# Kernel optimization log

Hardware: AMD Instinct MI355X
Metric: run time of the kernel (lower is better)

The kernel has to match this reference:

```python
import jax, jax.numpy as jnp
import numpy as np

U = 1024   # units
DK = 1024  # attention inner dim (dk)
B, T, D = 64, 128, 256


def setup_inputs() -> dict:
    key = jax.random.key(0)
    ks = jax.random.split(key, 20)
    s_w = 0.02   # dense-kernel init scale
    s_a = 0.03   # ~glorot for (1, dk) attention vectors
    inp = {
        'x': jax.random.normal(ks[0], (B, T, D), jnp.float32),
        'kernel': jax.random.normal(ks[1], (D, 5 * U), jnp.float32) * s_w,
        'recurrent_kernel': jax.random.normal(ks[2], (U, 5 * U), jnp.float32) * s_w,
        'cell_kernel': jax.random.normal(ks[3], (U, 5 * U), jnp.float32) * s_w,
        'bias': jnp.zeros((5 * U,), jnp.float32),
        'aggregation': jax.random.normal(ks[4], (3 * U, U), jnp.float32) * s_w,
    }
    att_names = ['up_att_downl', 'up_att_downr', 'up_att_randl', 'up_att_randr',
                 'rand_att_upl', 'rand_att_upr', 'rand_att_downl', 'rand_att_downr',
                 'down_att_upl', 'down_att_upr', 'down_att_randl', 'down_att_randr']
    for i, n in enumerate(att_names):
        inp[n] = jax.random.normal(ks[5 + i], (1, DK), jnp.float32) * s_a
    return inp


def _cumsoftmax_l2r(x):
    return jnp.cumsum(jax.nn.softmax(x, axis=-1), axis=-1)


def _cumsoftmax_r2l(x):
    # reverse, softmax+cumsum, reverse back (softmax is permutation-equivariant)
    return jnp.cumsum(jax.nn.softmax(x, axis=-1)[..., ::-1], axis=-1)[..., ::-1]


def _forward(x, kernel, recurrent_kernel, cell_kernel, bias, aggregation,
             up_att_downl, up_att_downr, up_att_randl, up_att_randr,
             rand_att_upl, rand_att_upr, rand_att_downl, rand_att_downr,
             down_att_upl, down_att_upr, down_att_randl, down_att_randr):
    # Rank-1 collapse of (v w_l)(u w_r)^T v chains: scalar = w_l . w_r
    s_ud = jnp.sum(up_att_downl * up_att_downr)
    s_ur = jnp.sum(up_att_randl * up_att_randr)
    s_ru = jnp.sum(rand_att_upl * rand_att_upr)
    s_rd = jnp.sum(rand_att_downl * rand_att_downr)
    s_du = jnp.sum(down_att_upl * down_att_upr)
    s_dr = jnp.sum(down_att_randl * down_att_randr)

    # precompute input projection for all timesteps: [T, B, 5U]
    xw = jnp.einsum('btd,dk->tbk', x, kernel) + bias

    def step(carry, xw_t):
        c, h = carry
        z = xw_t + h @ recurrent_kernel + c @ cell_kernel  # [B, 5U]
        up = _cumsoftmax_l2r(z[:, :U])
        down = _cumsoftmax_r2l(z[:, U:2 * U])
        rand = z[:, 2 * U:3 * U]
        du = jnp.sum(down * up, axis=-1, keepdims=True)    # <down, up> per batch
        ru = jnp.sum(rand * up, axis=-1, keepdims=True)
        dr = jnp.sum(down * rand, axis=-1, keepdims=True)
        O1 = jax.nn.sigmoid(s_ud * up * du) + jax.nn.sigmoid(s_ur * up * ru)
        O2 = jax.nn.sigmoid(s_ru * rand * ru) + jax.nn.sigmoid(s_rd * rand * dr)
        O3 = jax.nn.sigmoid(s_du * down * du) + jax.nn.sigmoid(s_dr * down * dr)
        f_gate = jax.nn.sigmoid(jnp.concatenate([O1, O2, O3], axis=-1) @ aggregation)
        i_gate = 1.0 - f_gate
        o_gate = z[:, 3 * U:4 * U]          # NOTE: no sigmoid in the original
        c_in = jnp.tanh(z[:, 4 * U:])
        c_new = f_gate * c + i_gate * c_in
        h_new = o_gate * jnp.tanh(c_new)
        return (c_new, h_new), h_new

    init = (jnp.zeros((x.shape[0], U), x.dtype), jnp.zeros((x.shape[0], U), x.dtype))
    _, hs = jax.lax.scan(step, init, xw)
    return jnp.transpose(hs, (1, 0, 2))  # return_sequences=True -> [B, T, U]


def reference(x, kernel, recurrent_kernel, cell_kernel, bias, aggregation,
              up_att_downl, up_att_downr, up_att_randl, up_att_randr,
              rand_att_upl, rand_att_upr, rand_att_downl, rand_att_downr,
              down_att_upl, down_att_upr, down_att_randl, down_att_randr):
    return _forward(x, kernel, recurrent_kernel, cell_kernel, bias, aggregation,
                    up_att_downl, up_att_downr, up_att_randl, up_att_randr,
                    rand_att_upl, rand_att_upr, rand_att_downl, rand_att_downr,
                    down_att_upl, down_att_upr, down_att_randl, down_att_randr)
```

## Files before the change

### kernel.cpp

```cpp
#include <hip/hip_runtime.h>
#include <hip/hip_bf16.h>


typedef short  bf16x8 __attribute__((ext_vector_type(8)));
typedef float  f32x4  __attribute__((ext_vector_type(4)));
typedef _Float16 f16;
typedef _Float16 f16x8 __attribute__((ext_vector_type(8)));
typedef __hip_bfloat16 bf16;
typedef unsigned long long u64;

#define U 1024
#define BATCH 64
#define TSTEPS 128
#define DIM 256
#define N5 5120
#define K2 2048

#define OFF_WRC   0u
#define OFF_KT    20971520u
#define OFF_AGGT  23592960u
#define OFF_XBF   29884416u
#define OFF_ZP    34078720u
#define OFF_ABUF  39321600u
#define OFF_C32   39845888u
#define OFF_OBUF  40108032u
#define OFF_SCAL  40501248u
#define OFF_CTR   40501504u
#define OFF_PB    OFF_KT

#define NBLK_A 160
#define NBLK_B 64
#define NBLK   224
#define FPAD   8

#define KT_OFF 131072

#define MFMA16(a,b,c)  __builtin_amdgcn_mfma_f32_16x16x32_bf16((a),(b),(c),0,0,0)
#define MFMA16H(a,b,c) __builtin_amdgcn_mfma_f32_16x16x32_f16((a),(b),(c),0,0,0)

__global__ __launch_bounds__(256) void k_xconv(const float* __restrict__ in,
                                               f16* __restrict__ o, int n4) {
    const int i = blockIdx.x * 256 + threadIdx.x;
    if (i < n4) {
        const float4 v = ((const float4*)in)[i];
        f16 tmp[4] = {(f16)v.x, (f16)v.y, (f16)v.z, (f16)v.w};
        ((uint2*)o)[i] = *(const uint2*)tmp;
    }
}

__global__ __launch_bounds__(256) void k_transpose_h(const float* __restrict__ in,
                                                     f16* __restrict__ out,
                                                     int C, int out_stride, int out_off) {
    __shared__ f16 tile[64][65];
    const int tc = blockIdx.x * 64, tr = blockIdx.y * 64;
    const int tx = threadIdx.x & 63, ty0 = threadIdx.x >> 6;
#pragma unroll
    for (int i = 0; i < 64; i += 4)
        tile[ty0 + i][tx] = (f16)(in[(tr + ty0 + i) * C + tc + tx]);
    __syncthreads();
#pragma unroll
    for (int i = 0; i < 64; i += 4)
        out[(tc + ty0 + i) * out_stride + out_off + tr + tx] = tile[tx][ty0 + i];
}

__global__ __launch_bounds__(256) void k_transpose_b(const float* __restrict__ in,
                                                     bf16* __restrict__ out,
                                                     int C, int out_stride, int out_off) {
    __shared__ bf16 tile[64][65];
    const int tc = blockIdx.x * 64, tr = blockIdx.y * 64;
    const int tx = threadIdx.x & 63, ty0 = threadIdx.x >> 6;
#pragma unroll
    for (int i = 0; i < 64; i += 4)
        tile[ty0 + i][tx] = __float2bfloat16(in[(tr + ty0 + i) * C + tc + tx]);
    __syncthreads();
#pragma unroll
    for (int i = 0; i < 64; i += 4)
        out[(tc + ty0 + i) * out_stride + out_off + tr + tx] = tile[tx][ty0 + i];
}

struct AttPtrs { const float* p[12]; };

__global__ __launch_bounds__(256) void k_scal(AttPtrs ap, float* __restrict__ scal) {
    __shared__ float red[256];
    const int tid = threadIdx.x;
    for (int q = 0; q < 6; ++q) {
        const float* l = ap.p[2 * q];
        const float* r = ap.p[2 * q + 1];
        float s = 0.f;
        for (int i = tid; i < 1024; i += 256)
            s += l[i] * r[i];
        red[tid] = s; __syncthreads();
        for (int o = 128; o > 0; o >>= 1) {
            if (tid < o) red[tid] += red[tid + o];
            __syncthreads();
        }
        if (tid == 0) scal[q] = red[0];
        __syncthreads();
    }
}

__device__ __forceinline__ float wave_sum(float v) {
#pragma unroll
    for (int o = 32; o > 0; o >>= 1) v += __shfl_xor(v, o, 64);
    return v;
}
__device__ __forceinline__ float wave_max(float v) {
#pragma unroll
    for (int o = 32; o > 0; o >>= 1) v = fmaxf(v, __shfl_xor(v, o, 64));
    return v;
}
__device__ __forceinline__ float wave_scan(float v, int lane) {
#pragma unroll
    for (int o = 1; o < 64; o <<= 1) {
        float n = __shfl_up(v, o, 64);
        if (lane >= o) v += n;
    }
    return v;
}
__device__ __forceinline__ float block_sum(float v, float* sm4, int w, int lane) {
    float s = wave_sum(v);
    if (lane == 0) sm4[w] = s;
    __syncthreads();
    float r = sm4[0] + sm4[1] + sm4[2] + sm4[3];
    __syncthreads();
    return r;
}
__device__ __forceinline__ float block_max(float v, float* sm4, int w, int lane) {
    float s = wave_max(v);
    if (lane == 0) sm4[w] = s;
    __syncthreads();
    float r = fmaxf(fmaxf(sm4[0], sm4[1]), fmaxf(sm4[2], sm4[3]));
    __syncthreads();
    return r;
}
__device__ __forceinline__ float block_scan(float v, float* sm4, int w, int lane, float* total) {
    float ws = wave_scan(v, lane);
    if (lane == 63) sm4[w] = ws;
    __syncthreads();
    float base = 0.f;
    if (w > 0) base += sm4[0];
    if (w > 1) base += sm4[1];
    if (w > 2) base += sm4[2];
    *total = sm4[0] + sm4[1] + sm4[2] + sm4[3];
    __syncthreads();
    return base + ws;
}
__device__ __forceinline__ float sigm(float x) { return 1.f / (1.f + __expf(-x)); }

__device__ __forceinline__ u64 ald64(const void* p) {
    return __hip_atomic_load((const u64*)p, __ATOMIC_RELAXED, __HIP_MEMORY_SCOPE_AGENT);
}
__device__ __forceinline__ bf16x8 ald16B(const bf16* p) {
    union { bf16x8 v; u64 u[2]; } r;
    r.u[0] = ald64(p);
    r.u[1] = ald64((const char*)p + 8);
    return r.v;
}
__device__ __forceinline__ f16x8 aldh16B(const f16* p) {
    union { f16x8 v; u64 u[2]; } r;
    r.u[0] = ald64(p);
    r.u[1] = ald64((const char*)p + 8);
    return r.v;
}
__device__ __forceinline__ f32x4 ald_f4(const float* p) {
    union { f32x4 v; u64 u[2]; } r;
    r.u[0] = ald64(p);
    r.u[1] = ald64(p + 2);
    return r.v;
}
__device__ __forceinline__ float ald_f(const float* p) {
    return __hip_atomic_load(p, __ATOMIC_RELAXED, __HIP_MEMORY_SCOPE_AGENT);
}
__device__ __forceinline__ void ast64(void* p, u64 v) {
    __hip_atomic_store((u64*)p, v, __ATOMIC_RELAXED, __HIP_MEMORY_SCOPE_AGENT);
}
__device__ __forceinline__ void ast32(void* p, unsigned v) {
    __hip_atomic_store((unsigned*)p, v, __ATOMIC_RELAXED, __HIP_MEMORY_SCOPE_AGENT);
}
__device__ __forceinline__ void ast_f(float* p, float v) {
    __hip_atomic_store(p, v, __ATOMIC_RELAXED, __HIP_MEMORY_SCOPE_AGENT);
}
__device__ __forceinline__ unsigned h16bits(f16 h) {
    unsigned short s; __builtin_memcpy(&s, &h, 2); return (unsigned)s;
}
__device__ __forceinline__ u64 packf2(float a, float b) {
    union { float f[2]; u64 u; } r; r.f[0] = a; r.f[1] = b; return r.u;
}

__device__ __forceinline__ void signal_flag(int* f, int v) {
    __syncthreads();
    if (threadIdx.x == 0)
        __hip_atomic_store(f, v, __ATOMIC_RELAXED, __HIP_MEMORY_SCOPE_AGENT);
}
__device__ __forceinline__ void wait_ge(const int* f, int n, int tgt) {
    if (threadIdx.x < 64) {
        for (;;) {
            int mn = 0x7fffffff;
            for (int i = threadIdx.x; i < n; i += 64) {
                const int v = __hip_atomic_load(f + i * FPAD, __ATOMIC_RELAXED,
                                                __HIP_MEMORY_SCOPE_AGENT);
                mn = v < mn ? v : mn;
            }
            if (__all(mn >= tgt)) break;
            __builtin_amdgcn_s_sleep(1);
        }
    }
    __syncthreads();
}

__device__ __forceinline__ bf16x8 lds_rd(const char* s, int nloc, int kb, int rs) {
    return *(const bf16x8*)(s + nloc * rs + (kb ^ ((nloc & 7) << 4)));
}
__device__ __forceinline__ f16x8 lds_rdh(const char* s, int nloc, int kb, int rs) {
    return *(const f16x8*)(s + nloc * rs + (kb ^ ((nloc & 7) << 4)));
}

__global__ __launch_bounds__(256, 1) void k_persist(
    const f16* __restrict__ xbf, const f16* __restrict__ kt,
    const f16* __restrict__ wrct, const bf16* __restrict__ aggt,
    float* __restrict__ zp, f16* __restrict__ abuf,
    float* __restrict__ c32, bf16* __restrict__ obuf,
    float* __restrict__ pbuf,
    const float* __restrict__ scal, const float* __restrict__ bias,
    float* __restrict__ out, int* __restrict__ ctr)
{
    __shared__ __align__(16) char smem[147456];
    __shared__ float sm4[4];

    const int bid = blockIdx.x, tid = threadIdx.x;
    const int w = tid >> 6, lane = tid & 63;
    const int ml = lane & 15, q = lane >> 4;
    int* fA = ctr;
    int* fB = ctr + 1280;
    int* fC = ctr + 1792;
    int* fP = ctr + 2304;

    if (bid < NBLK_A) {
        const int cg = bid >> 2;
        const int kq = bid & 3;
        const int n0 = cg * 128;
        const int kwbase = (kq < 2) ? kq * 512 : 1024 + (kq - 2) * 512;
        const int kA0 = (kq & 1) * 512;

        for (int i = 0; i < 32; ++i) {
            const int cid = i * 256 + tid;
            const int row = cid >> 6, k = (cid & 63) * 8;
            f16x8 v = *(const f16x8*)(wrct + (size_t)(n0 + row) * K2 + kwbase + k);
            *(f16x8*)(smem + row * 1024 + ((k * 2) ^ ((row & 7) << 4))) = v;
        }
        for (int i = 0; i < 4; ++i) {
            const int cid = i * 256 + tid;
            const int row = cid >> 3, k = (cid & 7) * 8;
            f16x8 v = *(const f16x8*)(kt + (size_t)(n0 + row) * DIM + kq * 64 + k);
            *(f16x8*)(smem + KT_OFF + row * 128 + ((k * 2) ^ ((row & 7) << 4))) = v;
        }
        __syncthreads();

        const int arow = w * 16 + ml;
        const f16* hP = abuf + (kq < 2 ? 0 : 1) * 65536 + arow * U + kA0;
        const f16* xrow = xbf + (size_t)arow * TSTEPS * DIM;
        float* zpq = zp + (size_t)kq * 64 * N5;
        int* fCmy = fC + ((kq & 1) * 32) * FPAD;

        for (int t = 0; t < TSTEPS; ++t) {
            const f16x8 ax0 = *(const f16x8*)(xrow + t * DIM + kq * 64 + q * 8);
            const f16x8 ax1 = *(const f16x8*)(xrow + t * DIM + kq * 64 + 32 + q * 8);

            wait_ge(fCmy, 32, t);

            f16x8 a[16];
#pragma unroll
            for (int i = 0; i < 16; ++i)
                a[i] = aldh16B(hP + i * 32 + q * 8);

            f32x4 acc[8];
#pragma unroll
            for (int i = 0; i < 8; ++i) acc[i] = (f32x4){0.f, 0.f, 0.f, 0.f};

#pragma unroll
            for (int cx = 0; cx < 2; ++cx) {
                const f16x8 axv = cx ? ax1 : ax0;
#pragma unroll
                for (int ct = 0; ct < 8; ++ct) {
                    const f16x8 b = lds_rdh(smem + KT_OFF, ct * 16 + ml, cx * 64 + q * 16, 128);
                    acc[ct] = MFMA16H(axv, b, acc[ct]);
                }
            }

#pragma unroll
            for (int i = 0; i < 16; ++i) {
                const int g = i >> 1, c = i & 1;
#pragma unroll
                for (int ct = 0; ct < 8; ++ct) {
                    const f16x8 b = lds_rdh(smem, ct * 16 + ml,
                                            g * 128 + c * 64 + q * 16, 1024);
                    acc[ct] = MFMA16H(a[i], b, acc[ct]);
                }
            }

#pragma unroll
            for (int ct = 0; ct < 8; ++ct)
#pragma unroll
                for (int r = 0; r < 4; ++r) {
                    const float v = acc[ct][r];
                    const float pv = __shfl_xor(v, 1, 64);
                    if (!(ml & 1)) {
                        const int row = w * 16 + q * 4 + r;
                        const int col = n0 + ct * 16 + ml;
                        ast64(&zpq[row * N5 + col], packf2(v, pv));
                    }
                }
            signal_flag(fA + bid * FPAD, t + 1);
        }
    } else {
        const int rb = bid - NBLK_A;
        const int cg = rb >> 2;
        const int kq2 = rb & 3;
        const int nst = cg * 64 + kq2 * 16;
        const int KO = kq2 * 768;

        for (int i = 0; i < 24; ++i) {
            const int cid = i * 256 + tid;
            const int nloc = cid / 96, kc = cid - nloc * 96;
            const int k = kc * 8;
            bf16x8 v = *(const bf16x8*)(aggt + (size_t)(cg * 64 + nloc) * 3072 + KO + k);
            *(bf16x8*)(smem + nloc * 1536 + ((k * 2) ^ ((nloc & 7) << 4))) = v;
        }
        __syncthreads();

        const float s_ud = scal[0], s_ur = scal[1], s_ru = scal[2],
                    s_rd = scal[3], s_du = scal[4], s_dr = scal[5];
        const int rowA = w * 16 + ml;
        const bf16* orow = obuf + rowA * 3072 + KO;
        float* cpriv = c32 + rb * 1024;

        for (int t = 0; t < TSTEPS; ++t) {
            wait_ge(fA, 96, t + 1);
            {
                f32x4 zu = {0.f,0.f,0.f,0.f}, zd = {0.f,0.f,0.f,0.f}, zn = {0.f,0.f,0.f,0.f};
#pragma unroll
                for (int kqi = 0; kqi < 4; ++kqi) {
                    const float* bp = zp + (size_t)kqi * 64 * N5 + rb * N5;
                    zu += ald_f4(bp + tid * 4);
                    zd += ald_f4(bp + U + tid * 4);
                    zn += ald_f4(bp + 2 * U + tid * 4);
                }
                zu += ((const f32x4*)bias)[tid];
                zd += ((const f32x4*)(bias + U))[tid];
                zn += ((const f32x4*)(bias + 2 * U))[tid];

                float mup = block_max(fmaxf(fmaxf(zu[0], zu[1]), fmaxf(zu[2], zu[3])), sm4, w, lane);
                const float e0 = __expf(zu[0] - mup), e1 = __expf(zu[1] - mup),
                            e2 = __expf(zu[2] - mup), e3 = __expf(zu[3] - mup);
                float totu;
                float inclu = block_scan(e0 + e1 + e2 + e3, sm4, w, lane, &totu);
                const float exclu = inclu - (e0 + e1 + e2 + e3);
                const float inv_u = 1.f / totu;
                const float u0 = (exclu + e0) * inv_u;
                const float u1 = (exclu + e0 + e1) * inv_u;
                const float u2 = (exclu + e0 + e1 + e2) * inv_u;
                const float u3 = (exclu + e0 + e1 + e2 + e3) * inv_u;

                float mdn = block_max(fmaxf(fmaxf(zd[0], zd[1]), fmaxf(zd[2], zd[3])), sm4, w, lane);
                const float f0 = __expf(zd[0] - mdn), f1 = __expf(zd[1] - mdn),
                            f2 = __expf(zd[2] - mdn), f3 = __expf(zd[3] - mdn);
                float totd;
                float incld = block_scan(f0 + f1 + f2 + f3, sm4, w, lane, &totd);
                const float excld = incld - (f0 + f1 + f2 + f3);
                const float inv_d = 1.f / totd;
                const float d0 = (totd - excld) * inv_d;
                const float d1 = (totd - excld - f0) * inv_d;
                const float d2 = (totd - excld - f0 - f1) * inv_d;
                const float d3 = (totd - excld - f0 - f1 - f2) * inv_d;

                const float du = block_sum(d0 * u0 + d1 * u1 + d2 * u2 + d3 * u3, sm4, w, lane);
                const float ru = block_sum(zn[0] * u0 + zn[1] * u1 + zn[2] * u2 + zn[3] * u3, sm4, w, lane);
                const float dr = block_sum(d0 * zn[0] + d1 * zn[1] + d2 * zn[2] + d3 * zn[3], sm4, w, lane);

                bf16* orw = obuf + rb * 3072;
                const int j0 = tid * 4;
                const float uu[4] = {u0, u1, u2, u3};
                const float dd[4] = {d0, d1, d2, d3};
                const float rr[4] = {zn[0], zn[1], zn[2], zn[3]};
                union { bf16 h[4]; u64 u; } p1, p2, p3;
#pragma unroll
                for (int i = 0; i < 4; ++i) {
                    p1.h[i] = __float2bfloat16(sigm(s_ud * uu[i] * du) + sigm(s_ur * uu[i] * ru));
                    p2.h[i] = __float2bfloat16(sigm(s_ru * rr[i] * ru) + sigm(s_rd * rr[i] * dr));
                    p3.h[i] = __float2bfloat16(sigm(s_du * dd[i] * du) + sigm(s_dr * dd[i] * dr));
                }
                ast64(orw + j0,         p1.u);
                ast64(orw + U + j0,     p2.u);
                ast64(orw + 2 * U + j0, p3.u);
            }
            signal_flag(fB + rb * FPAD, t + 1);

            wait_ge(fA + 96 * FPAD, 64, t + 1);
            float z3v[4], z4v[4];
            {
                const int col = nst + ml;
                const int r0 = w * 16 + q * 4;
#pragma unroll
                for (int r = 0; r < 4; ++r) {
                    z3v[r] = bias[3 * U + col];
                    z4v[r] = bias[4 * U + col];
#pragma unroll
                    for (int kqi = 0; kqi < 4; ++kqi) {
                        const float* zr = zp + (size_t)kqi * 64 * N5 + (size_t)(r0 + r) * N5;
                        z3v[r] += ald_f(zr + 3 * U + col);
                        z4v[r] += ald_f(zr + 4 * U + col);
                    }
                }
            }
            wait_ge(fB, NBLK_B, t + 1);
            {
                f32x4 acc[4];
#pragma unroll
                for (int i = 0; i < 4; ++i) acc[i] = (f32x4){0.f, 0.f, 0.f, 0.f};
                bf16x8 ob[3][8];
#pragma unroll
                for (int G = 0; G < 3; ++G)
#pragma unroll
                    for (int j = 0; j < 8; ++j)
                        ob[G][j] = ald16B(orow + (G * 8 + j) * 32 + q * 8);
#pragma unroll
                for (int g = 0; g < 3; ++g)
#pragma unroll
                    for (int j = 0; j < 8; ++j) {
                        const int kc = g * 8 + j;
#pragma unroll
                        for (int ct = 0; ct < 4; ++ct) {
                            const bf16x8 b = lds_rd(smem, ct * 16 + ml, kc * 64 + q * 16, 1536);
                            acc[ct] = MFMA16(ob[g][j], b, acc[ct]);
                        }
                    }
#pragma unroll
                for (int ct = 0; ct < 4; ++ct)
#pragma unroll
                    for (int r = 0; r < 4; ++r) {
                        const int row = w * 16 + q * 4 + r;
                        ast_f(&pbuf[(((size_t)cg * 64 + row) * 64 + ct * 16 + ml) * 4 + kq2],
                              acc[ct][r]);
                    }
            }
            signal_flag(fP + rb * FPAD, t + 1);
            wait_ge(fP + cg * 4 * FPAD, 4, t + 1);
            float hns[4];
            {
                const int col = nst + ml;
                const int r0 = w * 16 + q * 4;
#pragma unroll
                for (int r = 0; r < 4; ++r) {
                    const int row = r0 + r;
                    const f32x4 pj = ald_f4(&pbuf[(((size_t)cg * 64 + row) * 64 + kq2 * 16 + ml) * 4]);
                    const float s = (pj[0] + pj[1]) + (pj[2] + pj[3]);
                    const float f = sigm(s);
                    const float cold = cpriv[row * 16 + ml];
                    const float cn = f * cold + (1.f - f) * tanhf(z4v[r]);
                    const float hn = z3v[r] * tanhf(cn);
                    cpriv[row * 16 + ml] = cn;
                    hns[r] = hn;
                    const f16 hhb = (f16)hn;
                    const f16 ccb = (f16)cn;
                    unsigned vh = h16bits(hhb), vc = h16bits(ccb);
                    const unsigned ph = (unsigned)__shfl_xor((int)vh, 1, 64);
                    const unsigned pc = (unsigned)__shfl_xor((int)vc, 1, 64);
                    if (!(ml & 1)) {
                        const int eo = row * U + col;
                        ast32((unsigned*)(abuf + 0 * 65536 + eo), vh | (ph << 16));
                        ast32((unsigned*)(abuf + 1 * 65536 + eo), vc | (pc << 16));
                    }
                }
            }
            signal_flag(fC + rb * FPAD, t + 1);
            {
                const int col = nst + ml;
                const int r0 = w * 16 + q * 4;
#pragma unroll
                for (int r = 0; r < 4; ++r)
                    out[((size_t)(r0 + r) * TSTEPS + t) * U + col] = hns[r];
            }
        }
    }
}

extern "C" void kernel_launch(void* const* d_in, const int* in_sizes, int n_in,
                              void* d_out, int out_size, void* d_ws, size_t ws_size,
                              hipStream_t stream) {
    (void)in_sizes; (void)n_in; (void)out_size; (void)ws_size;
    const float* x    = (const float*)d_in[0];
    const float* Wk   = (const float*)d_in[1];
    const float* Wr   = (const float*)d_in[2];
    const float* Wc   = (const float*)d_in[3];
    const float* bias = (const float*)d_in[4];
    const float* agg  = (const float*)d_in[5];

    char* ws = (char*)d_ws;
    f16*   wrct = (f16*)(ws + OFF_WRC);
    f16*   kt   = (f16*)(ws + OFF_KT);
    bf16*  aggt = (bf16*)(ws + OFF_AGGT);
    f16*   xbf  = (f16*)(ws + OFF_XBF);
    float* zp   = (float*)(ws + OFF_ZP);
    f16*   abuf = (f16*)(ws + OFF_ABUF);
    float* c32  = (float*)(ws + OFF_C32);
    bf16*  obuf = (bf16*)(ws + OFF_OBUF);
    float* pbuf = (float*)(ws + OFF_PB);
    float* scal = (float*)(ws + OFF_SCAL);
    int*   ctr  = (int*)(ws + OFF_CTR);
    float* out  = (float*)d_out;

    hipMemsetAsync(abuf, 0, 2 * 65536 * sizeof(f16), stream);
    hipMemsetAsync(c32, 0, BATCH * U * sizeof(float), stream);
    hipMemsetAsync(ctr, 0, 12288, stream);

    k_xconv<<<(BATCH * TSTEPS * DIM / 4 + 255) / 256, 256, 0, stream>>>(x, xbf, BATCH * TSTEPS * DIM / 4);
    k_transpose_h<<<dim3(5120 / 64, 1024 / 64), 256, 0, stream>>>(Wr, wrct, 5120, 2048, 0);
    k_transpose_h<<<dim3(5120 / 64, 1024 / 64), 256, 0, stream>>>(Wc, wrct, 5120, 2048, 1024);
    k_transpose_h<<<dim3(5120 / 64, 256 / 64),  256, 0, stream>>>(Wk, kt,   5120, 256, 0);
    k_transpose_b<<<dim3(1024 / 64, 3072 / 64), 256, 0, stream>>>(agg, aggt, 1024, 3072, 0);

    AttPtrs ap;
    for (int i = 0; i < 12; ++i) ap.p[i] = (const float*)d_in[6 + i];
    k_scal<<<1, 256, 0, stream>>>(ap, scal);

    k_persist<<<NBLK, 256, 0, stream>>>(xbf, kt, wrct, aggt, zp, abuf, c32,
                                        obuf, pbuf, scal, bias, out, ctr);
}
```

Baseline: 3.363 ms.

## Remove split-K partial buffer for aggregation GEMM; each block owns full K for 16 columns

The aggregation matmul used to split K four ways across blocks, write partials to a global buffer, then run a second grid-level flag wait before summing them. Now each B-block keeps all 3072 K rows for its 16 output columns in LDS and computes the whole dot product itself, using two accumulators and a rotating register prefetch of obuf. Each wave waits only on the 16 producer flags for its own rows rather than on all blocks. This removes one global round trip and one cross-block barrier per timestep, at the cost of a larger serial MFMA chain and more obuf loads per block.

```diff
diff --git a/kernel.cpp b/kernel.cpp
--- a/kernel.cpp
+++ b/kernel.cpp
@@ -26,13 +26,13 @@
 #define OFF_OBUF  40108032u
 #define OFF_SCAL  40501248u
 #define OFF_CTR   40501504u
-#define OFF_PB    OFF_KT
 
 #define NBLK_A 160
 #define NBLK_B 64
 #define NBLK   224
 #define FPAD   8
 
+#define RS_B 6144
 #define KT_OFF 131072
 
 #define MFMA16(a,b,c)  __builtin_amdgcn_mfma_f32_16x16x32_bf16((a),(b),(c),0,0,0)
@@ -177,9 +177,6 @@
 __device__ __forceinline__ void ast32(void* p, unsigned v) {
     __hip_atomic_store((unsigned*)p, v, __ATOMIC_RELAXED, __HIP_MEMORY_SCOPE_AGENT);
 }
-__device__ __forceinline__ void ast_f(float* p, float v) {
-    __hip_atomic_store(p, v, __ATOMIC_RELAXED, __HIP_MEMORY_SCOPE_AGENT);
-}
 __device__ __forceinline__ unsigned h16bits(f16 h) {
     unsigned short s; __builtin_memcpy(&s, &h, 2); return (unsigned)s;
 }
@@ -207,6 +204,19 @@
     }
     __syncthreads();
 }
+__device__ __forceinline__ void wave_wait_ge(const int* f, int n, int tgt) {
+    const int lane = threadIdx.x & 63;
+    for (;;) {
+        int mn = 0x7fffffff;
+        for (int i = lane; i < n; i += 64) {
+            const int v = __hip_atomic_load(f + i * FPAD, __ATOMIC_RELAXED,
+                                            __HIP_MEMORY_SCOPE_AGENT);
+            mn = v < mn ? v : mn;
+        }
+        if (__all(mn >= tgt)) break;
+        __builtin_amdgcn_s_sleep(1);
+    }
+}
 
 __device__ __forceinline__ bf16x8 lds_rd(const char* s, int nloc, int kb, int rs) {
     return *(const bf16x8*)(s + nloc * rs + (kb ^ ((nloc & 7) << 4)));
@@ -220,7 +230,6 @@
     const f16* __restrict__ wrct, const bf16* __restrict__ aggt,
     float* __restrict__ zp, f16* __restrict__ abuf,
     float* __restrict__ c32, bf16* __restrict__ obuf,
-    float* __restrict__ pbuf,
     const float* __restrict__ scal, const float* __restrict__ bias,
     float* __restrict__ out, int* __restrict__ ctr)
 {
@@ -233,7 +242,6 @@
     int* fA = ctr;
     int* fB = ctr + 1280;
     int* fC = ctr + 1792;
-    int* fP = ctr + 2304;
 
     if (bid < NBLK_A) {
         const int cg = bid >> 2;
@@ -314,25 +322,26 @@
         }
     } else {
         const int rb = bid - NBLK_A;
-        const int cg = rb >> 2;
-        const int kq2 = rb & 3;
-        const int nst = cg * 64 + kq2 * 16;
-        const int KO = kq2 * 768;
-
+        const int n0b = rb * 16;
         for (int i = 0; i < 24; ++i) {
             const int cid = i * 256 + tid;
-            const int nloc = cid / 96, kc = cid - nloc * 96;
+            const int nloc = cid / 384, kc = cid - nloc * 384;
             const int k = kc * 8;
-            bf16x8 v = *(const bf16x8*)(aggt + (size_t)(cg * 64 + nloc) * 3072 + KO + k);
-            *(bf16x8*)(smem + nloc * 1536 + ((k * 2) ^ ((nloc & 7) << 4))) = v;
+            bf16x8 v = *(const bf16x8*)(aggt + (size_t)(n0b + nloc) * 3072 + k);
+            *(bf16x8*)(smem + nloc * RS_B + ((k * 2) ^ ((nloc & 7) << 4))) = v;
         }
         __syncthreads();
 
         const float s_ud = scal[0], s_ur = scal[1], s_ru = scal[2],
                     s_rd = scal[3], s_du = scal[4], s_dr = scal[5];
         const int rowA = w * 16 + ml;
-        const bf16* orow = obuf + rowA * 3072 + KO;
+        const bf16* orow = obuf + rowA * 3072;
         float* cpriv = c32 + rb * 1024;
+
+#define LOADO(G, BUF) do { _Pragma("unroll") \
+        for (int j_ = 0; j_ < 8; ++j_) \
+            ob[BUF][j_] = ald16B(orow + ((G) * 8 + j_) * 32 + q * 8); \
+        } while (0)
 
         for (int t = 0; t < TSTEPS; ++t) {
             wait_ge(fA, 96, t + 1);
@@ -398,7 +407,7 @@
             wait_ge(fA + 96 * FPAD, 64, t + 1);
             float z3v[4], z4v[4];
             {
-                const int col = nst + ml;
+                const int col = n0b + ml;
                 const int r0 = w * 16 + q * 4;
 #pragma unroll
                 for (int r = 0; r < 4; ++r) {
@@ -412,49 +421,33 @@
                     }
                 }
             }
-            wait_ge(fB, NBLK_B, t + 1);
-            {
-                f32x4 acc[4];
-#pragma unroll
-                for (int i = 0; i < 4; ++i) acc[i] = (f32x4){0.f, 0.f, 0.f, 0.f};
-                bf16x8 ob[3][8];
-#pragma unroll
-                for (int G = 0; G < 3; ++G)
-#pragma unroll
-                    for (int j = 0; j < 8; ++j)
-                        ob[G][j] = ald16B(orow + (G * 8 + j) * 32 + q * 8);
-#pragma unroll
-                for (int g = 0; g < 3; ++g)
-#pragma unroll
-                    for (int j = 0; j < 8; ++j) {
-                        const int kc = g * 8 + j;
-#pragma unroll
-                        for (int ct = 0; ct < 4; ++ct) {
-                            const bf16x8 b = lds_rd(smem, ct * 16 + ml, kc * 64 + q * 16, 1536);
-                            acc[ct] = MFMA16(ob[g][j], b, acc[ct]);
-                        }
-                    }
-#pragma unroll
-                for (int ct = 0; ct < 4; ++ct)
-#pragma unroll
-                    for (int r = 0; r < 4; ++r) {
-                        const int row = w * 16 + q * 4 + r;
-                        ast_f(&pbuf[(((size_t)cg * 64 + row) * 64 + ct * 16 + ml) * 4 + kq2],
-                              acc[ct][r]);
-                    }
-            }
-            signal_flag(fP + rb * FPAD, t + 1);
-            wait_ge(fP + cg * 4 * FPAD, 4, t + 1);
+            wave_wait_ge(fB + (w * 16) * FPAD, 16, t + 1);
             float hns[4];
             {
-                const int col = nst + ml;
+                f32x4 p0 = {0.f, 0.f, 0.f, 0.f}, p1 = {0.f, 0.f, 0.f, 0.f};
+                bf16x8 ob[4][8];
+                LOADO(0, 0);
+                LOADO(1, 1);
+                LOADO(2, 2);
+#pragma unroll
+                for (int g = 0; g < 12; ++g) {
+                    if (g < 9) LOADO(g + 3, (g + 3) & 3);
+#pragma unroll
+                    for (int j = 0; j < 8; ++j) {
+                        const int ch = g * 8 + j;
+                        const int kb = ch * 64 + q * 16;
+                        const bf16x8 b = lds_rd(smem, ml, kb, RS_B);
+                        if (j & 1) p1 = MFMA16(ob[g & 3][j], b, p1);
+                        else       p0 = MFMA16(ob[g & 3][j], b, p0);
+                    }
+                }
+                const f32x4 accv = p0 + p1;
+                const int col = n0b + ml;
                 const int r0 = w * 16 + q * 4;
 #pragma unroll
                 for (int r = 0; r < 4; ++r) {
                     const int row = r0 + r;
-                    const f32x4 pj = ald_f4(&pbuf[(((size_t)cg * 64 + row) * 64 + kq2 * 16 + ml) * 4]);
-                    const float s = (pj[0] + pj[1]) + (pj[2] + pj[3]);
-                    const float f = sigm(s);
+                    const float f = sigm(accv[r]);
                     const float cold = cpriv[row * 16 + ml];
                     const float cn = f * cold + (1.f - f) * tanhf(z4v[r]);
                     const float hn = z3v[r] * tanhf(cn);
@@ -474,13 +467,14 @@
             }
             signal_flag(fC + rb * FPAD, t + 1);
             {
-                const int col = nst + ml;
+                const int col = n0b + ml;
                 const int r0 = w * 16 + q * 4;
 #pragma unroll
                 for (int r = 0; r < 4; ++r)
                     out[((size_t)(r0 + r) * TSTEPS + t) * U + col] = hns[r];
             }
         }
+#undef LOADO
     }
 }
 
@@ -504,7 +498,6 @@
     f16*   abuf = (f16*)(ws + OFF_ABUF);
     float* c32  = (float*)(ws + OFF_C32);
     bf16*  obuf = (bf16*)(ws + OFF_OBUF);
-    float* pbuf = (float*)(ws + OFF_PB);
     float* scal = (float*)(ws + OFF_SCAL);
     int*   ctr  = (int*)(ws + OFF_CTR);
     float* out  = (float*)d_out;
@@ -524,5 +517,5 @@
     k_scal<<<1, 256, 0, stream>>>(ap, scal);
 
     k_persist<<<NBLK, 256, 0, stream>>>(xbf, kt, wrct, aggt, zp, abuf, c32,
-                                        obuf, pbuf, scal, bias, out, ctr);
-}
+                                        obuf, scal, bias, out, ctr);
+}
```

New measurement: 5.672 ms. 68.6% more time.

## Store inter-block partial sums in fp16 and merge the two A-stage waits

Applied to the files above, without the earlier changes.

Moves the inter-block partial buffers (z partials, aggregation partials, attention outputs) and the aggregation weights from fp32/bf16 to fp16, with fp16 MFMA for the aggregation matmul. This halves the global traffic through the synchronising buffers on the per-timestep critical path. The B blocks now wait once for all A blocks and load the output and cell-input gate partials early, instead of waiting separately on a second group. The cost is lower precision in the partial sums and a wider single wait, which may lose some overlap.

```diff
diff --git a/kernel.cpp b/kernel.cpp
--- a/kernel.cpp
+++ b/kernel.cpp
@@ -2,11 +2,9 @@
 #include <hip/hip_bf16.h>
 
 
-typedef short  bf16x8 __attribute__((ext_vector_type(8)));
 typedef float  f32x4  __attribute__((ext_vector_type(4)));
 typedef _Float16 f16;
 typedef _Float16 f16x8 __attribute__((ext_vector_type(8)));
-typedef __hip_bfloat16 bf16;
 typedef unsigned long long u64;
 
 #define U 1024
@@ -35,7 +33,6 @@
 
 #define KT_OFF 131072
 
-#define MFMA16(a,b,c)  __builtin_amdgcn_mfma_f32_16x16x32_bf16((a),(b),(c),0,0,0)
 #define MFMA16H(a,b,c) __builtin_amdgcn_mfma_f32_16x16x32_f16((a),(b),(c),0,0,0)
 
 __global__ __launch_bounds__(256) void k_xconv(const float* __restrict__ in,
@@ -57,21 +54,6 @@
 #pragma unroll
     for (int i = 0; i < 64; i += 4)
         tile[ty0 + i][tx] = (f16)(in[(tr + ty0 + i) * C + tc + tx]);
-    __syncthreads();
-#pragma unroll
-    for (int i = 0; i < 64; i += 4)
-        out[(tc + ty0 + i) * out_stride + out_off + tr + tx] = tile[tx][ty0 + i];
-}
-
-__global__ __launch_bounds__(256) void k_transpose_b(const float* __restrict__ in,
-                                                     bf16* __restrict__ out,
-                                                     int C, int out_stride, int out_off) {
-    __shared__ bf16 tile[64][65];
-    const int tc = blockIdx.x * 64, tr = blockIdx.y * 64;
-    const int tx = threadIdx.x & 63, ty0 = threadIdx.x >> 6;
-#pragma unroll
-    for (int i = 0; i < 64; i += 4)
-        tile[ty0 + i][tx] = __float2bfloat16(in[(tr + ty0 + i) * C + tc + tx]);
     __syncthreads();
 #pragma unroll
     for (int i = 0; i < 64; i += 4)
@@ -150,11 +132,8 @@
 __device__ __forceinline__ u64 ald64(const void* p) {
     return __hip_atomic_load((const u64*)p, __ATOMIC_RELAXED, __HIP_MEMORY_SCOPE_AGENT);
 }
-__device__ __forceinline__ bf16x8 ald16B(const bf16* p) {
-    union { bf16x8 v; u64 u[2]; } r;
-    r.u[0] = ald64(p);
-    r.u[1] = ald64((const char*)p + 8);
-    return r.v;
+__device__ __forceinline__ unsigned ald32(const void* p) {
+    return __hip_atomic_load((const unsigned*)p, __ATOMIC_RELAXED, __HIP_MEMORY_SCOPE_AGENT);
 }
 __device__ __forceinline__ f16x8 aldh16B(const f16* p) {
     union { f16x8 v; u64 u[2]; } r;
@@ -162,29 +141,21 @@
     r.u[1] = ald64((const char*)p + 8);
     return r.v;
 }
-__device__ __forceinline__ f32x4 ald_f4(const float* p) {
-    union { f32x4 v; u64 u[2]; } r;
-    r.u[0] = ald64(p);
-    r.u[1] = ald64(p + 2);
-    return r.v;
-}
-__device__ __forceinline__ float ald_f(const float* p) {
-    return __hip_atomic_load(p, __ATOMIC_RELAXED, __HIP_MEMORY_SCOPE_AGENT);
-}
 __device__ __forceinline__ void ast64(void* p, u64 v) {
     __hip_atomic_store((u64*)p, v, __ATOMIC_RELAXED, __HIP_MEMORY_SCOPE_AGENT);
 }
 __device__ __forceinline__ void ast32(void* p, unsigned v) {
     __hip_atomic_store((unsigned*)p, v, __ATOMIC_RELAXED, __HIP_MEMORY_SCOPE_AGENT);
 }
-__device__ __forceinline__ void ast_f(float* p, float v) {
-    __hip_atomic_store(p, v, __ATOMIC_RELAXED, __HIP_MEMORY_SCOPE_AGENT);
+__device__ __forceinline__ void ast16(void* p, unsigned short v) {
+    __hip_atomic_store((unsigned short*)p, v, __ATOMIC_RELAXED, __HIP_MEMORY_SCOPE_AGENT);
 }
 __device__ __forceinline__ unsigned h16bits(f16 h) {
     unsigned short s; __builtin_memcpy(&s, &h, 2); return (unsigned)s;
 }
-__device__ __forceinline__ u64 packf2(float a, float b) {
-    union { float f[2]; u64 u; } r; r.f[0] = a; r.f[1] = b; return r.u;
+__device__ __forceinline__ float h16f(unsigned bits) {
+    unsigned short s = (unsigned short)bits; f16 h;
+    __builtin_memcpy(&h, &s, 2); return (float)h;
 }
 
 __device__ __forceinline__ void signal_flag(int* f, int v) {
@@ -208,19 +179,16 @@
     __syncthreads();
 }
 
-__device__ __forceinline__ bf16x8 lds_rd(const char* s, int nloc, int kb, int rs) {
-    return *(const bf16x8*)(s + nloc * rs + (kb ^ ((nloc & 7) << 4)));
-}
 __device__ __forceinline__ f16x8 lds_rdh(const char* s, int nloc, int kb, int rs) {
     return *(const f16x8*)(s + nloc * rs + (kb ^ ((nloc & 7) << 4)));
 }
 
 __global__ __launch_bounds__(256, 1) void k_persist(
     const f16* __restrict__ xbf, const f16* __restrict__ kt,
-    const f16* __restrict__ wrct, const bf16* __restrict__ aggt,
-    float* __restrict__ zp, f16* __restrict__ abuf,
-    float* __restrict__ c32, bf16* __restrict__ obuf,
-    float* __restrict__ pbuf,
+    const f16* __restrict__ wrct, const f16* __restrict__ aggt,
+    f16* __restrict__ zp, f16* __restrict__ abuf,
+    float* __restrict__ c32, f16* __restrict__ obuf,
+    f16* __restrict__ pbuf,
     const float* __restrict__ scal, const float* __restrict__ bias,
     float* __restrict__ out, int* __restrict__ ctr)
 {
@@ -259,7 +227,7 @@
         const int arow = w * 16 + ml;
         const f16* hP = abuf + (kq < 2 ? 0 : 1) * 65536 + arow * U + kA0;
         const f16* xrow = xbf + (size_t)arow * TSTEPS * DIM;
-        float* zpq = zp + (size_t)kq * 64 * N5;
+        f16* zpq = zp + (size_t)kq * 64 * N5;
         int* fCmy = fC + ((kq & 1) * 32) * FPAD;
 
         for (int t = 0; t < TSTEPS; ++t) {
@@ -302,12 +270,14 @@
             for (int ct = 0; ct < 8; ++ct)
 #pragma unroll
                 for (int r = 0; r < 4; ++r) {
-                    const float v = acc[ct][r];
-                    const float pv = __shfl_xor(v, 1, 64);
-                    if (!(ml & 1)) {
+                    const unsigned b0 = h16bits((f16)acc[ct][r]);
+                    const unsigned p01 = b0 | ((unsigned)__shfl_xor((int)b0, 1, 64) << 16);
+                    const u64 p = (u64)p01
+                                | ((u64)(unsigned)__shfl_xor((int)p01, 2, 64) << 32);
+                    if (!(ml & 3)) {
                         const int row = w * 16 + q * 4 + r;
                         const int col = n0 + ct * 16 + ml;
-                        ast64(&zpq[row * N5 + col], packf2(v, pv));
+                        ast64(&zpq[row * N5 + col], p);
                     }
                 }
             signal_flag(fA + bid * FPAD, t + 1);
@@ -323,27 +293,54 @@
             const int cid = i * 256 + tid;
             const int nloc = cid / 96, kc = cid - nloc * 96;
             const int k = kc * 8;
-            bf16x8 v = *(const bf16x8*)(aggt + (size_t)(cg * 64 + nloc) * 3072 + KO + k);
-            *(bf16x8*)(smem + nloc * 1536 + ((k * 2) ^ ((nloc & 7) << 4))) = v;
+            f16x8 v = *(const f16x8*)(aggt + (size_t)(cg * 64 + nloc) * 3072 + KO + k);
+            *(f16x8*)(smem + nloc * 1536 + ((k * 2) ^ ((nloc & 7) << 4))) = v;
         }
         __syncthreads();
 
         const float s_ud = scal[0], s_ur = scal[1], s_ru = scal[2],
                     s_rd = scal[3], s_du = scal[4], s_dr = scal[5];
         const int rowA = w * 16 + ml;
-        const bf16* orow = obuf + rowA * 3072 + KO;
+        const f16* orow = obuf + rowA * 3072 + KO;
         float* cpriv = c32 + rb * 1024;
 
+#define LOADO(G, BUF) do { _Pragma("unroll") \
+        for (int j_ = 0; j_ < 8; ++j_) \
+            ob[BUF][j_] = aldh16B(orow + ((G) * 8 + j_) * 32 + q * 8); \
+        } while (0)
+
+        const int colst = nst + ml;
+        const int cest = colst & ~1;
+        const int r0 = w * 16 + q * 4;
+
         for (int t = 0; t < TSTEPS; ++t) {
-            wait_ge(fA, 96, t + 1);
+            wait_ge(fA, NBLK_A, t + 1);
+
+            unsigned r3[4][4], r4[4][4];
+#pragma unroll
+            for (int r = 0; r < 4; ++r)
+#pragma unroll
+                for (int kqi = 0; kqi < 4; ++kqi) {
+                    const f16* zr = zp + (size_t)kqi * 64 * N5 + (size_t)(r0 + r) * N5;
+                    r3[r][kqi] = ald32(zr + 3 * U + cest);
+                    r4[r][kqi] = ald32(zr + 4 * U + cest);
+                }
+
             {
                 f32x4 zu = {0.f,0.f,0.f,0.f}, zd = {0.f,0.f,0.f,0.f}, zn = {0.f,0.f,0.f,0.f};
 #pragma unroll
                 for (int kqi = 0; kqi < 4; ++kqi) {
-                    const float* bp = zp + (size_t)kqi * 64 * N5 + rb * N5;
-                    zu += ald_f4(bp + tid * 4);
-                    zd += ald_f4(bp + U + tid * 4);
-                    zn += ald_f4(bp + 2 * U + tid * 4);
+                    const f16* bp = zp + (size_t)kqi * 64 * N5 + rb * N5;
+                    union { u64 u; f16 h[4]; } cu, cd, cn_;
+                    cu.u  = ald64(bp + tid * 4);
+                    cd.u  = ald64(bp + U + tid * 4);
+                    cn_.u = ald64(bp + 2 * U + tid * 4);
+#pragma unroll
+                    for (int e = 0; e < 4; ++e) {
+                        zu[e] += (float)cu.h[e];
+                        zd[e] += (float)cd.h[e];
+                        zn[e] += (float)cn_.h[e];
+                    }
                 }
                 zu += ((const f32x4*)bias)[tid];
                 zd += ((const f32x4*)(bias + U))[tid];
@@ -377,17 +374,17 @@
                 const float ru = block_sum(zn[0] * u0 + zn[1] * u1 + zn[2] * u2 + zn[3] * u3, sm4, w, lane);
                 const float dr = block_sum(d0 * zn[0] + d1 * zn[1] + d2 * zn[2] + d3 * zn[3], sm4, w, lane);
 
-                bf16* orw = obuf + rb * 3072;
+                f16* orw = obuf + rb * 3072;
                 const int j0 = tid * 4;
                 const float uu[4] = {u0, u1, u2, u3};
                 const float dd[4] = {d0, d1, d2, d3};
                 const float rr[4] = {zn[0], zn[1], zn[2], zn[3]};
-                union { bf16 h[4]; u64 u; } p1, p2, p3;
+                union { f16 h[4]; u64 u; } p1, p2, p3;
 #pragma unroll
                 for (int i = 0; i < 4; ++i) {
-                    p1.h[i] = __float2bfloat16(sigm(s_ud * uu[i] * du) + sigm(s_ur * uu[i] * ru));
-                    p2.h[i] = __float2bfloat16(sigm(s_ru * rr[i] * ru) + sigm(s_rd * rr[i] * dr));
-                    p3.h[i] = __float2bfloat16(sigm(s_du * dd[i] * du) + sigm(s_dr * dd[i] * dr));
+                    p1.h[i] = (f16)(sigm(s_ud * uu[i] * du) + sigm(s_ur * uu[i] * ru));
+                    p2.h[i] = (f16)(sigm(s_ru * rr[i] * ru) + sigm(s_rd * rr[i] * dr));
+                    p3.h[i] = (f16)(sigm(s_du * dd[i] * du) + sigm(s_dr * dd[i] * dr));
                 }
                 ast64(orw + j0,         p1.u);
                 ast64(orw + U + j0,     p2.u);
@@ -395,21 +392,18 @@
             }
             signal_flag(fB + rb * FPAD, t + 1);
 
-            wait_ge(fA + 96 * FPAD, 64, t + 1);
             float z3v[4], z4v[4];
             {
-                const int col = nst + ml;
-                const int r0 = w * 16 + q * 4;
+                const int hi = (colst & 1) * 16;
 #pragma unroll
                 for (int r = 0; r < 4; ++r) {
-                    z3v[r] = bias[3 * U + col];
-                    z4v[r] = bias[4 * U + col];
+                    float s3 = bias[3 * U + colst], s4 = bias[4 * U + colst];
 #pragma unroll
                     for (int kqi = 0; kqi < 4; ++kqi) {
-                        const float* zr = zp + (size_t)kqi * 64 * N5 + (size_t)(r0 + r) * N5;
-                        z3v[r] += ald_f(zr + 3 * U + col);
-                        z4v[r] += ald_f(zr + 4 * U + col);
+                        s3 += h16f(r3[r][kqi] >> hi);
+                        s4 += h16f(r4[r][kqi] >> hi);
                     }
+                    z3v[r] = s3; z4v[r] = s4;
                 }
             }
             wait_ge(fB, NBLK_B, t + 1);
@@ -417,12 +411,12 @@
                 f32x4 acc[4];
 #pragma unroll
                 for (int i = 0; i < 4; ++i) acc[i] = (f32x4){0.f, 0.f, 0.f, 0.f};
-                bf16x8 ob[3][8];
+                f16x8 ob[3][8];
 #pragma unroll
                 for (int G = 0; G < 3; ++G)
 #pragma unroll
                     for (int j = 0; j < 8; ++j)
-                        ob[G][j] = ald16B(orow + (G * 8 + j) * 32 + q * 8);
+                        ob[G][j] = aldh16B(orow + (G * 8 + j) * 32 + q * 8);
 #pragma unroll
                 for (int g = 0; g < 3; ++g)
 #pragma unroll
@@ -430,8 +424,8 @@
                         const int kc = g * 8 + j;
 #pragma unroll
                         for (int ct = 0; ct < 4; ++ct) {
-                            const bf16x8 b = lds_rd(smem, ct * 16 + ml, kc * 64 + q * 16, 1536);
-                            acc[ct] = MFMA16(ob[g][j], b, acc[ct]);
+                            const f16x8 b = lds_rdh(smem, ct * 16 + ml, kc * 64 + q * 16, 1536);
+                            acc[ct] = MFMA16H(ob[g][j], b, acc[ct]);
                         }
                     }
 #pragma unroll
@@ -439,34 +433,32 @@
 #pragma unroll
                     for (int r = 0; r < 4; ++r) {
                         const int row = w * 16 + q * 4 + r;
-                        ast_f(&pbuf[(((size_t)cg * 64 + row) * 64 + ct * 16 + ml) * 4 + kq2],
-                              acc[ct][r]);
+                        ast16(&pbuf[(((size_t)cg * 64 + row) * 64 + ct * 16 + ml) * 4 + kq2],
+                              (unsigned short)h16bits((f16)acc[ct][r]));
                     }
             }
             signal_flag(fP + rb * FPAD, t + 1);
             wait_ge(fP + cg * 4 * FPAD, 4, t + 1);
             float hns[4];
             {
-                const int col = nst + ml;
-                const int r0 = w * 16 + q * 4;
 #pragma unroll
                 for (int r = 0; r < 4; ++r) {
                     const int row = r0 + r;
-                    const f32x4 pj = ald_f4(&pbuf[(((size_t)cg * 64 + row) * 64 + kq2 * 16 + ml) * 4]);
-                    const float s = (pj[0] + pj[1]) + (pj[2] + pj[3]);
+                    union { u64 u; f16 h[4]; } pj;
+                    pj.u = ald64(&pbuf[(((size_t)cg * 64 + row) * 64 + kq2 * 16 + ml) * 4]);
+                    const float s = ((float)pj.h[0] + (float)pj.h[1])
+                                  + ((float)pj.h[2] + (float)pj.h[3]);
                     const float f = sigm(s);
                     const float cold = cpriv[row * 16 + ml];
                     const float cn = f * cold + (1.f - f) * tanhf(z4v[r]);
                     const float hn = z3v[r] * tanhf(cn);
                     cpriv[row * 16 + ml] = cn;
                     hns[r] = hn;
-                    const f16 hhb = (f16)hn;
-                    const f16 ccb = (f16)cn;
-                    unsigned vh = h16bits(hhb), vc = h16bits(ccb);
+                    unsigned vh = h16bits((f16)hn), vc = h16bits((f16)cn);
                     const unsigned ph = (unsigned)__shfl_xor((int)vh, 1, 64);
                     const unsigned pc = (unsigned)__shfl_xor((int)vc, 1, 64);
                     if (!(ml & 1)) {
-                        const int eo = row * U + col;
+                        const int eo = row * U + colst;
                         ast32((unsigned*)(abuf + 0 * 65536 + eo), vh | (ph << 16));
                         ast32((unsigned*)(abuf + 1 * 65536 + eo), vc | (pc << 16));
                     }
@@ -474,13 +466,12 @@
             }
             signal_flag(fC + rb * FPAD, t + 1);
             {
-                const int col = nst + ml;
-                const int r0 = w * 16 + q * 4;
 #pragma unroll
                 for (int r = 0; r < 4; ++r)
-                    out[((size_t)(r0 + r) * TSTEPS + t) * U + col] = hns[r];
-            }
-        }
+                    out[((size_t)(r0 + r) * TSTEPS + t) * U + colst] = hns[r];
+            }
+        }
+#undef LOADO
     }
 }
 
@@ -498,13 +489,13 @@
     char* ws = (char*)d_ws;
     f16*   wrct = (f16*)(ws + OFF_WRC);
     f16*   kt   = (f16*)(ws + OFF_KT);
-    bf16*  aggt = (bf16*)(ws + OFF_AGGT);
+    f16*   aggt = (f16*)(ws + OFF_AGGT);
     f16*   xbf  = (f16*)(ws + OFF_XBF);
-    float* zp   = (float*)(ws + OFF_ZP);
+    f16*   zp   = (f16*)(ws + OFF_ZP);
     f16*   abuf = (f16*)(ws + OFF_ABUF);
     float* c32  = (float*)(ws + OFF_C32);
-    bf16*  obuf = (bf16*)(ws + OFF_OBUF);
-    float* pbuf = (float*)(ws + OFF_PB);
+    f16*   obuf = (f16*)(ws + OFF_OBUF);
+    f16*   pbuf = (f16*)(ws + OFF_PB);
     float* scal = (float*)(ws + OFF_SCAL);
     int*   ctr  = (int*)(ws + OFF_CTR);
     float* out  = (float*)d_out;
@@ -517,7 +508,7 @@
     k_transpose_h<<<dim3(5120 / 64, 1024 / 64), 256, 0, stream>>>(Wr, wrct, 5120, 2048, 0);
     k_transpose_h<<<dim3(5120 / 64, 1024 / 64), 256, 0, stream>>>(Wc, wrct, 5120, 2048, 1024);
     k_transpose_h<<<dim3(5120 / 64, 256 / 64),  256, 0, stream>>>(Wk, kt,   5120, 256, 0);
-    k_transpose_b<<<dim3(1024 / 64, 3072 / 64), 256, 0, stream>>>(agg, aggt, 1024, 3072, 0);
+    k_transpose_h<<<dim3(1024 / 64, 3072 / 64), 256, 0, stream>>>(agg, aggt, 1024, 3072, 0);
 
     AttPtrs ap;
     for (int i = 0; i < 12; ++i) ap.p[i] = (const float*)d_in[6 + i];
```

New measurement: 3.587 ms. +6.7%, slower.

## Replace block-level flags with per-wave flags for finer-grained inter-block sync

Applied to the files above, without the earlier changes.

Cross-block progress flags now live per wavefront instead of per block. Each wave signals its own flag after draining its stores and waits only on the flags of the producer waves whose rows it consumes, which removes several __syncthreads barriers from the recurrent step. The aim is to cut the serialized signal/wait latency on the per-timestep critical path. The cost is more flags to poll and a larger counter region to clear. Correctness now depends on the wave-to-row mapping being exact, and visibility relies on vmcnt waits plus relaxed atomics.

```diff
diff --git a/kernel.cpp b/kernel.cpp
--- a/kernel.cpp
+++ b/kernel.cpp
@@ -192,12 +192,17 @@
     if (threadIdx.x == 0)
         __hip_atomic_store(f, v, __ATOMIC_RELAXED, __HIP_MEMORY_SCOPE_AGENT);
 }
-__device__ __forceinline__ void wait_ge(const int* f, int n, int tgt) {
+__device__ __forceinline__ void wave_signal(int* f, int v) {
+    asm volatile("s_waitcnt vmcnt(0)" ::: "memory");
+    if ((threadIdx.x & 63) == 0)
+        __hip_atomic_store(f, v, __ATOMIC_RELAXED, __HIP_MEMORY_SCOPE_AGENT);
+}
+__device__ __forceinline__ void wait_ge_s(const int* f0, int n, int stride, int tgt) {
     if (threadIdx.x < 64) {
         for (;;) {
             int mn = 0x7fffffff;
             for (int i = threadIdx.x; i < n; i += 64) {
-                const int v = __hip_atomic_load(f + i * FPAD, __ATOMIC_RELAXED,
+                const int v = __hip_atomic_load(f0 + i * stride, __ATOMIC_RELAXED,
                                                 __HIP_MEMORY_SCOPE_AGENT);
                 mn = v < mn ? v : mn;
             }
@@ -206,6 +211,19 @@
         }
     }
     __syncthreads();
+}
+__device__ __forceinline__ void wave_wait_s(const int* f0, int n, int stride, int tgt) {
+    const int lane = threadIdx.x & 63;
+    for (;;) {
+        int mn = 0x7fffffff;
+        for (int i = lane; i < n; i += 64) {
+            const int v = __hip_atomic_load(f0 + i * stride, __ATOMIC_RELAXED,
+                                            __HIP_MEMORY_SCOPE_AGENT);
+            mn = v < mn ? v : mn;
+        }
+        if (__all(mn >= tgt)) break;
+        __builtin_amdgcn_s_sleep(1);
+    }
 }
 
 __device__ __forceinline__ bf16x8 lds_rd(const char* s, int nloc, int kb, int rs) {
@@ -230,10 +248,10 @@
     const int bid = blockIdx.x, tid = threadIdx.x;
     const int w = tid >> 6, lane = tid & 63;
     const int ml = lane & 15, q = lane >> 4;
-    int* fA = ctr;
-    int* fB = ctr + 1280;
-    int* fC = ctr + 1792;
-    int* fP = ctr + 2304;
+    int* fAw = ctr;
+    int* fB  = ctr + 5120;
+    int* fCw = ctr + 5632;
+    int* fPw = ctr + 7680;
 
     if (bid < NBLK_A) {
         const int cg = bid >> 2;
@@ -260,13 +278,15 @@
         const f16* hP = abuf + (kq < 2 ? 0 : 1) * 65536 + arow * U + kA0;
         const f16* xrow = xbf + (size_t)arow * TSTEPS * DIM;
         float* zpq = zp + (size_t)kq * 64 * N5;
-        int* fCmy = fC + ((kq & 1) * 32) * FPAD;
+        const int rb0 = (kq & 1) * 32;
+        int* fCmy = fCw + (rb0 * 4 + w) * FPAD;
+        int* fAmy = fAw + (bid * 4 + w) * FPAD;
 
         for (int t = 0; t < TSTEPS; ++t) {
             const f16x8 ax0 = *(const f16x8*)(xrow + t * DIM + kq * 64 + q * 8);
             const f16x8 ax1 = *(const f16x8*)(xrow + t * DIM + kq * 64 + 32 + q * 8);
 
-            wait_ge(fCmy, 32, t);
+            wave_wait_s(fCmy, 32, 4 * FPAD, t);
 
             f16x8 a[16];
 #pragma unroll
@@ -310,7 +330,7 @@
                         ast64(&zpq[row * N5 + col], packf2(v, pv));
                     }
                 }
-            signal_flag(fA + bid * FPAD, t + 1);
+            wave_signal(fAmy, t + 1);
         }
     } else {
         const int rb = bid - NBLK_A;
@@ -333,9 +353,10 @@
         const int rowA = w * 16 + ml;
         const bf16* orow = obuf + rowA * 3072 + KO;
         float* cpriv = c32 + rb * 1024;
+        const int wv = rb >> 4;
 
         for (int t = 0; t < TSTEPS; ++t) {
-            wait_ge(fA, 96, t + 1);
+            wait_ge_s(fAw + wv * FPAD, 96, 4 * FPAD, t + 1);
             {
                 f32x4 zu = {0.f,0.f,0.f,0.f}, zd = {0.f,0.f,0.f,0.f}, zn = {0.f,0.f,0.f,0.f};
 #pragma unroll
@@ -395,7 +416,7 @@
             }
             signal_flag(fB + rb * FPAD, t + 1);
 
-            wait_ge(fA + 96 * FPAD, 64, t + 1);
+            wave_wait_s(fAw + (96 * 4 + w) * FPAD, 64, 4 * FPAD, t + 1);
             float z3v[4], z4v[4];
             {
                 const int col = nst + ml;
@@ -412,7 +433,7 @@
                     }
                 }
             }
-            wait_ge(fB, NBLK_B, t + 1);
+            wave_wait_s(fB + (w * 16) * FPAD, 16, FPAD, t + 1);
             {
                 f32x4 acc[4];
 #pragma unroll
@@ -443,8 +464,8 @@
                               acc[ct][r]);
                     }
             }
-            signal_flag(fP + rb * FPAD, t + 1);
-            wait_ge(fP + cg * 4 * FPAD, 4, t + 1);
+            wave_signal(fPw + (rb * 4 + w) * FPAD, t + 1);
+            wave_wait_s(fPw + (cg * 16 + w) * FPAD, 4, 4 * FPAD, t + 1);
             float hns[4];
             {
                 const int col = nst + ml;
@@ -472,7 +493,7 @@
                     }
                 }
             }
-            signal_flag(fC + rb * FPAD, t + 1);
+            wave_signal(fCw + (rb * 4 + w) * FPAD, t + 1);
             {
                 const int col = nst + ml;
                 const int r0 = w * 16 + q * 4;
@@ -511,7 +532,7 @@
 
     hipMemsetAsync(abuf, 0, 2 * 65536 * sizeof(f16), stream);
     hipMemsetAsync(c32, 0, BATCH * U * sizeof(float), stream);
-    hipMemsetAsync(ctr, 0, 12288, stream);
+    hipMemsetAsync(ctr, 0, 40960, stream);
 
     k_xconv<<<(BATCH * TSTEPS * DIM / 4 + 255) / 256, 256, 0, stream>>>(x, xbf, BATCH * TSTEPS * DIM / 4);
     k_transpose_h<<<dim3(5120 / 64, 1024 / 64), 256, 0, stream>>>(Wr, wrct, 5120, 2048, 0);
```

Result: slower. 3.559 ms (+5.8%).
